# Kernel tuning notes

Hardware: AMD Instinct MI355X
Metric: run time of the kernel (lower is better)

Reference implementation:

```python
import jax, jax.numpy as jnp
import numpy as np

# bitsandbytes NF4 codebook (16 values)
NF4_TABLE = jnp.array([
    -1.0, -0.6961928009986877, -0.5250730514526367, -0.39491748809814453,
    -0.28444138169288635, -0.18477343022823334, -0.09105003625154495, 0.0,
    0.07958029955625534, 0.16093020141124725, 0.24611230194568634,
    0.33791524171829224, 0.44070982933044434, 0.5626170039176941,
    0.6989939212799072, 1.0], dtype=jnp.float32)
BLOCK = 64  # bitsandbytes default quantization blocksize


def dequant_nf4(codes, absmax):
    # codes: [out, in] int codebook indices; absmax: [out, in//BLOCK] per-block scales
    out_f, in_f = codes.shape
    w = NF4_TABLE[codes].reshape(out_f, in_f // BLOCK, BLOCK) * absmax[:, :, None]
    return w.reshape(out_f, in_f)


def setup_inputs() -> dict:
    key = jax.random.key(0)
    ks = jax.random.split(key, 7)
    dim, hidden = 4096, 11008
    B, S = 2, 2048
    x = jax.random.normal(ks[0], (B, S, dim), dtype=jnp.float32)
    w1_codes = jax.random.randint(ks[1], (hidden, dim), 0, 16, dtype=jnp.int32)
    w1_absmax = jax.random.uniform(ks[2], (hidden, dim // BLOCK), dtype=jnp.float32) * 0.05
    w2_codes = jax.random.randint(ks[3], (dim, hidden), 0, 16, dtype=jnp.int32)
    w2_absmax = jax.random.uniform(ks[4], (dim, hidden // BLOCK), dtype=jnp.float32) * 0.05
    w3_codes = jax.random.randint(ks[5], (hidden, dim), 0, 16, dtype=jnp.int32)
    w3_absmax = jax.random.uniform(ks[6], (hidden, dim // BLOCK), dtype=jnp.float32) * 0.05
    return {"x": x,
            "w1_codes": w1_codes, "w1_absmax": w1_absmax,
            "w2_codes": w2_codes, "w2_absmax": w2_absmax,
            "w3_codes": w3_codes, "w3_absmax": w3_absmax}


def reference(x, w1_codes, w1_absmax, w2_codes, w2_absmax, w3_codes, w3_absmax):
    # SwiGLU: w2(silu(w1(x)) * w3(x)) with NF4-dequantized weights, no bias
    W1 = dequant_nf4(w1_codes, w1_absmax)  # [hidden, dim]
    W3 = dequant_nf4(w3_codes, w3_absmax)  # [hidden, dim]
    W2 = dequant_nf4(w2_codes, w2_absmax)  # [dim, hidden]
    h = jax.nn.silu(jnp.einsum('bsd,hd->bsh', x, W1)) * jnp.einsum('bsd,hd->bsh', x, W3)
    return jnp.einsum('bsh,dh->bsd', h, W2)
```

## Files before the change

### kernel.cpp

```cpp
#include <hip/hip_runtime.h>
#include <hip/hip_bf16.h>
#include <stdint.h>

#define DIM   4096
#define HID   11008
#define MTOK  4096
#define NELW  (HID * DIM)

typedef __bf16 bf16x8 __attribute__((ext_vector_type(8)));
typedef float  f32x4  __attribute__((ext_vector_type(4)));
using gptr_t = const __attribute__((address_space(1))) void*;
using lptr_t = __attribute__((address_space(3))) void*;

__device__ __forceinline__ float bf2f(unsigned short u) {
    unsigned int t = ((unsigned int)u) << 16;
    float f; __builtin_memcpy(&f, &t, 4); return f;
}
__device__ __forceinline__ unsigned short f2bf(float f) {
    unsigned int x; __builtin_memcpy(&x, &f, 4);
    x += 0x7fffu + ((x >> 16) & 1u);
    return (unsigned short)(x >> 16);
}

__device__ __constant__ float NF4_TAB[16] = {
    -1.0f, -0.6961928009986877f, -0.5250730514526367f, -0.39491748809814453f,
    -0.28444138169288635f, -0.18477343022823334f, -0.09105003625154495f, 0.0f,
    0.07958029955625534f, 0.16093020141124725f, 0.24611230194568634f,
    0.33791524171829224f, 0.44070982933044434f, 0.5626170039176941f,
    0.6989939212799072f, 1.0f};

__global__ __launch_bounds__(256) void dequant_nf4_k(
    const int* __restrict__ codes, const float* __restrict__ absmax,
    unsigned short* __restrict__ out)
{
    long base = ((long)blockIdx.x * 256 + threadIdx.x) * 8;
    float tv = NF4_TAB[threadIdx.x & 15];
    int4 c0 = *(const int4*)(codes + base);
    int4 c1 = *(const int4*)(codes + base + 4);
    float s = absmax[base >> 6];
    union { uint4 q; unsigned short u[8]; } o;
    o.u[0] = f2bf(__shfl(tv, c0.x) * s);
    o.u[1] = f2bf(__shfl(tv, c0.y) * s);
    o.u[2] = f2bf(__shfl(tv, c0.z) * s);
    o.u[3] = f2bf(__shfl(tv, c0.w) * s);
    o.u[4] = f2bf(__shfl(tv, c1.x) * s);
    o.u[5] = f2bf(__shfl(tv, c1.y) * s);
    o.u[6] = f2bf(__shfl(tv, c1.z) * s);
    o.u[7] = f2bf(__shfl(tv, c1.w) * s);
    *(uint4*)(out + base) = o.q;
}

__global__ __launch_bounds__(256) void cast_f32_bf16_k(
    const float* __restrict__ in, unsigned short* __restrict__ out)
{
    long base = ((long)blockIdx.x * 256 + threadIdx.x) * 8;
    float4 a = *(const float4*)(in + base);
    float4 b = *(const float4*)(in + base + 4);
    union { uint4 q; unsigned short u[8]; } o;
    o.u[0] = f2bf(a.x); o.u[1] = f2bf(a.y); o.u[2] = f2bf(a.z); o.u[3] = f2bf(a.w);
    o.u[4] = f2bf(b.x); o.u[5] = f2bf(b.y); o.u[6] = f2bf(b.z); o.u[7] = f2bf(b.w);
    *(uint4*)(out + base) = o.q;
}

template<int MODE>
__global__ __launch_bounds__(512, 2) void gemm256_k(
    const unsigned short* __restrict__ A, const unsigned short* __restrict__ B,
    void* __restrict__ Cout, int M, int N, int K)
{
    __shared__ __align__(16) unsigned short lds[2][2][2][128 * 64];

    const int tid = threadIdx.x;
    const int w = tid >> 6, lane = tid & 63;
    const int wm = w >> 2, wn = w & 3;
    const int lrow = lane & 15, hi = lane >> 4;
    const int key = lrow & 7;

    const int nbm = M >> 8, nbn = N >> 8;
    const int cpx = (nbm * nbn) >> 3;
    int swz = ((int)blockIdx.x & 7) * cpx + ((int)blockIdx.x >> 3);
    const int bm = swz % nbm, bn = swz / nbm;

    const long ldK = K;
    const int srow = tid >> 3;
    const int scol = ((tid & 7) ^ (srow & 7)) * 8;
    const unsigned short* gA = A + ((long)(bm * 256 + srow)) * ldK + scol;
    const unsigned short* gB = B + ((long)(bn * 256 + srow)) * ldK + scol;

    f32x4 acc[8][4];
    #pragma unroll
    for (int m = 0; m < 8; ++m)
        #pragma unroll
        for (int n = 0; n < 4; ++n) acc[m][n] = f32x4{0.f, 0.f, 0.f, 0.f};

    bf16x8 a0[4][2], a1[4][2], b0[2][2], b1[2][2];

    auto STAGE = [&](int kt, int h, int b) {
        const unsigned short* src = ((h >> 1) ? gB : gA)
            + (long)((h & 1) * 128) * ldK + (long)kt * 64;
        char* dst = (char*)&lds[b][h >> 1][h & 1][0] + w * 1024;
        __builtin_amdgcn_global_load_lds((gptr_t)src, (lptr_t)dst, 16, 0, 0);
        __builtin_amdgcn_global_load_lds((gptr_t)(src + (long)64 * ldK),
                                         (lptr_t)(dst + 8192), 16, 0, 0);
    };
    auto LDA = [&](bf16x8 (&fr)[4][2], int which, int b) {
        const unsigned short* base = &lds[b][0][wm][0];
        #pragma unroll
        for (int m = 0; m < 4; ++m)
            #pragma unroll
            for (int ks = 0; ks < 2; ++ks)
                fr[m][ks] = *(const bf16x8*)(base + (which * 64 + m * 16 + lrow) * 64
                                             + (((ks * 4 + hi) ^ key) * 8));
    };
    auto LDB = [&](bf16x8 (&fr)[2][2], int which, int b) {
        const unsigned short* base = &lds[b][1][wn >> 1][0];
        #pragma unroll
        for (int n = 0; n < 2; ++n)
            #pragma unroll
            for (int ks = 0; ks < 2; ++ks)
                fr[n][ks] = *(const bf16x8*)(base + ((wn & 1) * 64 + (which * 2 + n) * 16 + lrow) * 64
                                             + (((ks * 4 + hi) ^ key) * 8));
    };
    auto MMA = [&](bf16x8 (&fa)[4][2], bf16x8 (&fb)[2][2], int mo, int no) {
        __builtin_amdgcn_s_setprio(1);
        #pragma unroll
        for (int m = 0; m < 4; ++m)
            #pragma unroll
            for (int n = 0; n < 2; ++n)
                #pragma unroll
                for (int ks = 0; ks < 2; ++ks)
                    acc[mo + m][no + n] = __builtin_amdgcn_mfma_f32_16x16x32_bf16(
                        fa[m][ks], fb[n][ks], acc[mo + m][no + n], 0, 0, 0);
        __builtin_amdgcn_s_setprio(0);
    };
    #define BAR() do { __builtin_amdgcn_s_barrier(); \
                       __builtin_amdgcn_sched_barrier(0xF); } while (0)

    const int NT = K >> 6;
    STAGE(0, 0, 0); STAGE(0, 1, 0); STAGE(0, 2, 0); STAGE(0, 3, 0);
    STAGE(1, 0, 1); STAGE(1, 1, 1);
    asm volatile("s_waitcnt vmcnt(4)" ::: "memory");
    BAR();
    LDA(a0, 0, 0);

    int cur = 0;
    for (int t = 0; t < NT - 1; ++t) {
        const int nb = cur ^ 1;
        const int tA = (t + 2 < NT) ? t + 2 : NT - 1;
        STAGE(t + 1, 2, nb);
        LDB(b0, 0, cur);
        BAR();
        MMA(a0, b0, 0, 0);
        BAR();
        STAGE(t + 1, 3, nb);
        LDA(a1, 1, cur);
        BAR();
        MMA(a1, b0, 4, 0);
        BAR();
        STAGE(tA, 0, cur);
        LDB(b1, 1, cur);
        BAR();
        MMA(a0, b1, 0, 2);
        asm volatile("s_waitcnt vmcnt(6)" ::: "memory");
        BAR();
        STAGE(tA, 1, cur);
        LDA(a0, 0, nb);
        BAR();
        MMA(a1, b1, 4, 2);
        asm volatile("s_waitcnt vmcnt(4)" ::: "memory");
        BAR();
        cur = nb;
    }
    LDB(b0, 0, cur);
    MMA(a0, b0, 0, 0);
    LDA(a1, 1, cur);
    MMA(a1, b0, 4, 0);
    LDB(b1, 1, cur);
    MMA(a0, b1, 0, 2);
    MMA(a1, b1, 4, 2);
    #undef BAR

    const int grow = bm * 256 + wm * 128 + hi * 4;
    const int gcol = bn * 256 + wn * 64 + lrow;
    if (MODE == 0) {
        float* C = (float*)Cout;
        #pragma unroll
        for (int m = 0; m < 8; ++m)
            #pragma unroll
            for (int n = 0; n < 4; ++n)
                #pragma unroll
                for (int r = 0; r < 4; ++r)
                    C[(long)(grow + m * 16 + r) * N + gcol + n * 16] = acc[m][n][r];
    } else if (MODE == 1) {
        unsigned short* C = (unsigned short*)Cout;
        #pragma unroll
        for (int m = 0; m < 8; ++m)
            #pragma unroll
            for (int n = 0; n < 4; ++n)
                #pragma unroll
                for (int r = 0; r < 4; ++r)
                    C[(long)(grow + m * 16 + r) * N + gcol + n * 16] = f2bf(acc[m][n][r]);
    } else {
        unsigned short* C = (unsigned short*)Cout;
        #pragma unroll
        for (int m = 0; m < 8; ++m)
            #pragma unroll
            for (int n = 0; n < 4; ++n)
                #pragma unroll
                for (int r = 0; r < 4; ++r) {
                    long idx = (long)(grow + m * 16 + r) * N + gcol + n * 16;
                    float h1v = bf2f(C[idx]);
                    float g = h1v / (1.0f + __expf(-h1v));
                    C[idx] = f2bf(g * acc[m][n][r]);
                }
    }
}

#define WS_NEEDED 304087040UL

extern "C" void kernel_launch(void* const* d_in, const int* in_sizes, int n_in,
                              void* d_out, int out_size, void* d_ws, size_t ws_size,
                              hipStream_t stream) {
    const float* x   = (const float*)d_in[0];
    const int*   w1c = (const int*)d_in[1];
    const float* w1a = (const float*)d_in[2];
    const int*   w2c = (const int*)d_in[3];
    const float* w2a = (const float*)d_in[4];
    const int*   w3c = (const int*)d_in[5];
    const float* w3a = (const float*)d_in[6];

    if (ws_size < WS_NEEDED) return;

    char* ws = (char*)d_ws;
    unsigned short* W1 = (unsigned short*)(ws);
    unsigned short* W3 = (unsigned short*)(ws + 90177536);
    unsigned short* Xb = (unsigned short*)(ws + 180355072);
    unsigned short* H1 = (unsigned short*)(ws + 213909504);

    const int wblk = NELW / (8 * 256);
    dequant_nf4_k<<<wblk, 256, 0, stream>>>(w1c, w1a, W1);
    dequant_nf4_k<<<wblk, 256, 0, stream>>>(w3c, w3a, W3);
    cast_f32_bf16_k<<<(MTOK * DIM) / (8 * 256), 256, 0, stream>>>(x, Xb);

    gemm256_k<1><<<(MTOK / 256) * (HID / 256), 512, 0, stream>>>(Xb, W1, H1, MTOK, HID, DIM);
    gemm256_k<2><<<(MTOK / 256) * (HID / 256), 512, 0, stream>>>(Xb, W3, H1, MTOK, HID, DIM);

    dequant_nf4_k<<<wblk, 256, 0, stream>>>(w2c, w2a, W1);

    gemm256_k<0><<<(MTOK / 256) * (DIM / 256), 512, 0, stream>>>(H1, W1, (float*)d_out, MTOK, DIM, HID);
}
```

Measured before the change: 1.165 ms.

## Use 32x32 MFMA tiles and overlap NF4 dequant with the GEMM grids

The GEMM inner loop moves from 16x16x32 to 32x32x16 bf16 MFMA instructions, with LDS fragment loads, accumulators and the epilogue row mapping rewritten to match. This cuts LDS reads per FLOP. The standalone W3 and W2 dequant launches are removed. Each is folded into the preceding GEMM launch as extra trailing grid-stride blocks, so the dequant runs alongside the GEMM tail instead of serially. The W1 dequant and the x-to-bf16 cast are merged into one launch. The risks are contention between dequant blocks and GEMM blocks, and correctness of the new 32x32 fragment layout.

```diff
diff --git a/kernel.cpp b/kernel.cpp
--- a/kernel.cpp
+++ b/kernel.cpp
@@ -8,7 +8,7 @@
 #define NELW  (HID * DIM)
 
 typedef __bf16 bf16x8 __attribute__((ext_vector_type(8)));
-typedef float  f32x4  __attribute__((ext_vector_type(4)));
+typedef float  f32x16 __attribute__((ext_vector_type(16)));
 using gptr_t = const __attribute__((address_space(1))) void*;
 using lptr_t = __attribute__((address_space(3))) void*;
 
@@ -29,12 +29,9 @@
     0.33791524171829224f, 0.44070982933044434f, 0.5626170039176941f,
     0.6989939212799072f, 1.0f};
 
-__global__ __launch_bounds__(256) void dequant_nf4_k(
-    const int* __restrict__ codes, const float* __restrict__ absmax,
-    unsigned short* __restrict__ out)
+__device__ __forceinline__ void dq8(const int* codes, const float* absmax,
+                                    unsigned short* out, long base, float tv)
 {
-    long base = ((long)blockIdx.x * 256 + threadIdx.x) * 8;
-    float tv = NF4_TAB[threadIdx.x & 15];
     int4 c0 = *(const int4*)(codes + base);
     int4 c1 = *(const int4*)(codes + base + 4);
     float s = absmax[base >> 6];
@@ -50,30 +47,55 @@
     *(uint4*)(out + base) = o.q;
 }
 
-__global__ __launch_bounds__(256) void cast_f32_bf16_k(
-    const float* __restrict__ in, unsigned short* __restrict__ out)
+#define W1BLK 22016
+#define PREBLK (W1BLK + (MTOK * DIM) / 2048)
+__global__ __launch_bounds__(256) void pre_k(
+    const int* __restrict__ w1c, const float* __restrict__ w1a,
+    unsigned short* __restrict__ W1,
+    const float* __restrict__ x, unsigned short* __restrict__ Xb)
 {
-    long base = ((long)blockIdx.x * 256 + threadIdx.x) * 8;
-    float4 a = *(const float4*)(in + base);
-    float4 b = *(const float4*)(in + base + 4);
-    union { uint4 q; unsigned short u[8]; } o;
-    o.u[0] = f2bf(a.x); o.u[1] = f2bf(a.y); o.u[2] = f2bf(a.z); o.u[3] = f2bf(a.w);
-    o.u[4] = f2bf(b.x); o.u[5] = f2bf(b.y); o.u[6] = f2bf(b.z); o.u[7] = f2bf(b.w);
-    *(uint4*)(out + base) = o.q;
+    float tv = NF4_TAB[threadIdx.x & 15];
+    if ((int)blockIdx.x < W1BLK) {
+        long base = ((long)blockIdx.x * 256 + threadIdx.x) * 8;
+        dq8(w1c, w1a, W1, base, tv);
+    } else {
+        long base = ((long)(blockIdx.x - W1BLK) * 256 + threadIdx.x) * 8;
+        float4 a = *(const float4*)(x + base);
+        float4 b = *(const float4*)(x + base + 4);
+        union { uint4 q; unsigned short u[8]; } o;
+        o.u[0] = f2bf(a.x); o.u[1] = f2bf(a.y); o.u[2] = f2bf(a.z); o.u[3] = f2bf(a.w);
+        o.u[4] = f2bf(b.x); o.u[5] = f2bf(b.y); o.u[6] = f2bf(b.z); o.u[7] = f2bf(b.w);
+        *(uint4*)(Xb + base) = o.q;
+    }
 }
 
 template<int MODE>
 __global__ __launch_bounds__(512, 2) void gemm256_k(
     const unsigned short* __restrict__ A, const unsigned short* __restrict__ B,
-    void* __restrict__ Cout, int M, int N, int K)
+    void* __restrict__ Cout, int M, int N, int K, int ngemm,
+    const int* __restrict__ dqc, const float* __restrict__ dqa,
+    unsigned short* __restrict__ dqo)
 {
     __shared__ __align__(16) unsigned short lds[2][2][2][128 * 64];
 
     const int tid = threadIdx.x;
-    const int w = tid >> 6, lane = tid & 63;
+    const int lane = tid & 63;
+
+    if ((int)blockIdx.x >= ngemm) {
+        if (!dqo) return;
+        const int b = (int)blockIdx.x - ngemm;
+        const int ndq = (int)gridDim.x - ngemm;
+        const long stride = (long)ndq * 512 * 8;
+        float tv = NF4_TAB[lane & 15];
+        for (long base = ((long)b * 512 + tid) * 8; base < (long)NELW; base += stride)
+            dq8(dqc, dqa, dqo, base, tv);
+        return;
+    }
+
+    const int w = tid >> 6;
     const int wm = w >> 2, wn = w & 3;
-    const int lrow = lane & 15, hi = lane >> 4;
-    const int key = lrow & 7;
+    const int l31 = lane & 31, l5 = lane >> 5;
+    const int key = lane & 7;
 
     const int nbm = M >> 8, nbn = N >> 8;
     const int cpx = (nbm * nbn) >> 3;
@@ -86,13 +108,15 @@
     const unsigned short* gA = A + ((long)(bm * 256 + srow)) * ldK + scol;
     const unsigned short* gB = B + ((long)(bn * 256 + srow)) * ldK + scol;
 
-    f32x4 acc[8][4];
+    f32x16 acc[4][2];
     #pragma unroll
-    for (int m = 0; m < 8; ++m)
-        #pragma unroll
-        for (int n = 0; n < 4; ++n) acc[m][n] = f32x4{0.f, 0.f, 0.f, 0.f};
-
-    bf16x8 a0[4][2], a1[4][2], b0[2][2], b1[2][2];
+    for (int m = 0; m < 4; ++m)
+        #pragma unroll
+        for (int n = 0; n < 2; ++n)
+            #pragma unroll
+            for (int r = 0; r < 16; ++r) acc[m][n][r] = 0.f;
+
+    bf16x8 aLo[2][4], aHi[2][4], bLo[4], bHi[4];
 
     auto STAGE = [&](int kt, int h, int b) {
         const unsigned short* src = ((h >> 1) ? gB : gA)
@@ -102,34 +126,34 @@
         __builtin_amdgcn_global_load_lds((gptr_t)(src + (long)64 * ldK),
                                          (lptr_t)(dst + 8192), 16, 0, 0);
     };
-    auto LDA = [&](bf16x8 (&fr)[4][2], int which, int b) {
+    auto LDA32 = [&](bf16x8 (&fr)[2][4], int which, int b) {
         const unsigned short* base = &lds[b][0][wm][0];
         #pragma unroll
-        for (int m = 0; m < 4; ++m)
-            #pragma unroll
-            for (int ks = 0; ks < 2; ++ks)
-                fr[m][ks] = *(const bf16x8*)(base + (which * 64 + m * 16 + lrow) * 64
-                                             + (((ks * 4 + hi) ^ key) * 8));
-    };
-    auto LDB = [&](bf16x8 (&fr)[2][2], int which, int b) {
+        for (int mt = 0; mt < 2; ++mt)
+            #pragma unroll
+            for (int ks = 0; ks < 4; ++ks) {
+                const int row = which * 64 + mt * 32 + l31;
+                fr[mt][ks] = *(const bf16x8*)(base + row * 64
+                                              + (((ks * 2 + l5) ^ key) * 8));
+            }
+    };
+    auto LDB32 = [&](bf16x8 (&fr)[4], int which, int b) {
         const unsigned short* base = &lds[b][1][wn >> 1][0];
         #pragma unroll
-        for (int n = 0; n < 2; ++n)
-            #pragma unroll
-            for (int ks = 0; ks < 2; ++ks)
-                fr[n][ks] = *(const bf16x8*)(base + ((wn & 1) * 64 + (which * 2 + n) * 16 + lrow) * 64
-                                             + (((ks * 4 + hi) ^ key) * 8));
-    };
-    auto MMA = [&](bf16x8 (&fa)[4][2], bf16x8 (&fb)[2][2], int mo, int no) {
+        for (int ks = 0; ks < 4; ++ks) {
+            const int row = (wn & 1) * 64 + which * 32 + l31;
+            fr[ks] = *(const bf16x8*)(base + row * 64
+                                      + (((ks * 2 + l5) ^ key) * 8));
+        }
+    };
+    auto MMA32 = [&](bf16x8 (&fa)[2][4], bf16x8 (&fb)[4], int mo, int no) {
         __builtin_amdgcn_s_setprio(1);
         #pragma unroll
-        for (int m = 0; m < 4; ++m)
-            #pragma unroll
-            for (int n = 0; n < 2; ++n)
-                #pragma unroll
-                for (int ks = 0; ks < 2; ++ks)
-                    acc[mo + m][no + n] = __builtin_amdgcn_mfma_f32_16x16x32_bf16(
-                        fa[m][ks], fb[n][ks], acc[mo + m][no + n], 0, 0, 0);
+        for (int mt = 0; mt < 2; ++mt)
+            #pragma unroll
+            for (int ks = 0; ks < 4; ++ks)
+                acc[mo + mt][no] = __builtin_amdgcn_mfma_f32_32x32x16_bf16(
+                    fa[mt][ks], fb[ks], acc[mo + mt][no], 0, 0, 0);
         __builtin_amdgcn_s_setprio(0);
     };
     #define BAR() do { __builtin_amdgcn_s_barrier(); \
@@ -140,82 +164,70 @@
     STAGE(1, 0, 1); STAGE(1, 1, 1);
     asm volatile("s_waitcnt vmcnt(4)" ::: "memory");
     BAR();
-    LDA(a0, 0, 0);
+    LDA32(aLo, 0, 0);
 
     int cur = 0;
     for (int t = 0; t < NT - 1; ++t) {
         const int nb = cur ^ 1;
         const int tA = (t + 2 < NT) ? t + 2 : NT - 1;
         STAGE(t + 1, 2, nb);
-        LDB(b0, 0, cur);
-        BAR();
-        MMA(a0, b0, 0, 0);
+        LDB32(bLo, 0, cur);
+        BAR();
+        MMA32(aLo, bLo, 0, 0);
         BAR();
         STAGE(t + 1, 3, nb);
-        LDA(a1, 1, cur);
-        BAR();
-        MMA(a1, b0, 4, 0);
+        LDA32(aHi, 1, cur);
+        BAR();
+        MMA32(aHi, bLo, 2, 0);
         BAR();
         STAGE(tA, 0, cur);
-        LDB(b1, 1, cur);
-        BAR();
-        MMA(a0, b1, 0, 2);
+        LDB32(bHi, 1, cur);
+        BAR();
+        MMA32(aLo, bHi, 0, 1);
         asm volatile("s_waitcnt vmcnt(6)" ::: "memory");
         BAR();
         STAGE(tA, 1, cur);
-        LDA(a0, 0, nb);
-        BAR();
-        MMA(a1, b1, 4, 2);
+        LDA32(aLo, 0, nb);
+        BAR();
+        MMA32(aHi, bHi, 2, 1);
         asm volatile("s_waitcnt vmcnt(4)" ::: "memory");
         BAR();
         cur = nb;
     }
-    LDB(b0, 0, cur);
-    MMA(a0, b0, 0, 0);
-    LDA(a1, 1, cur);
-    MMA(a1, b0, 4, 0);
-    LDB(b1, 1, cur);
-    MMA(a0, b1, 0, 2);
-    MMA(a1, b1, 4, 2);
+    LDB32(bLo, 0, cur);
+    MMA32(aLo, bLo, 0, 0);
+    LDA32(aHi, 1, cur);
+    MMA32(aHi, bLo, 2, 0);
+    LDB32(bHi, 1, cur);
+    MMA32(aLo, bHi, 0, 1);
+    MMA32(aHi, bHi, 2, 1);
     #undef BAR
 
-    const int grow = bm * 256 + wm * 128 + hi * 4;
-    const int gcol = bn * 256 + wn * 64 + lrow;
-    if (MODE == 0) {
-        float* C = (float*)Cout;
-        #pragma unroll
-        for (int m = 0; m < 8; ++m)
-            #pragma unroll
-            for (int n = 0; n < 4; ++n)
-                #pragma unroll
-                for (int r = 0; r < 4; ++r)
-                    C[(long)(grow + m * 16 + r) * N + gcol + n * 16] = acc[m][n][r];
-    } else if (MODE == 1) {
-        unsigned short* C = (unsigned short*)Cout;
-        #pragma unroll
-        for (int m = 0; m < 8; ++m)
-            #pragma unroll
-            for (int n = 0; n < 4; ++n)
-                #pragma unroll
-                for (int r = 0; r < 4; ++r)
-                    C[(long)(grow + m * 16 + r) * N + gcol + n * 16] = f2bf(acc[m][n][r]);
-    } else {
-        unsigned short* C = (unsigned short*)Cout;
-        #pragma unroll
-        for (int m = 0; m < 8; ++m)
-            #pragma unroll
-            for (int n = 0; n < 4; ++n)
-                #pragma unroll
-                for (int r = 0; r < 4; ++r) {
-                    long idx = (long)(grow + m * 16 + r) * N + gcol + n * 16;
+    const int grow0 = bm * 256 + wm * 128 + l5 * 4;
+    const int gcol0 = bn * 256 + wn * 64 + l31;
+    #pragma unroll
+    for (int mt = 0; mt < 4; ++mt)
+        #pragma unroll
+        for (int nt = 0; nt < 2; ++nt)
+            #pragma unroll
+            for (int r = 0; r < 16; ++r) {
+                const int row = grow0 + mt * 32 + (r & 3) + 8 * (r >> 2);
+                const long idx = (long)row * N + gcol0 + nt * 32;
+                if (MODE == 0) {
+                    ((float*)Cout)[idx] = acc[mt][nt][r];
+                } else if (MODE == 1) {
+                    ((unsigned short*)Cout)[idx] = f2bf(acc[mt][nt][r]);
+                } else {
+                    unsigned short* C = (unsigned short*)Cout;
                     float h1v = bf2f(C[idx]);
                     float g = h1v / (1.0f + __expf(-h1v));
-                    C[idx] = f2bf(g * acc[m][n][r]);
+                    C[idx] = f2bf(g * acc[mt][nt][r]);
                 }
-    }
+            }
 }
 
 #define WS_NEEDED 304087040UL
+#define DQBLK 512
 
 extern "C" void kernel_launch(void* const* d_in, const int* in_sizes, int n_in,
                               void* d_out, int out_size, void* d_ws, size_t ws_size,
@@ -236,15 +248,15 @@
     unsigned short* Xb = (unsigned short*)(ws + 180355072);
     unsigned short* H1 = (unsigned short*)(ws + 213909504);
 
-    const int wblk = NELW / (8 * 256);
-    dequant_nf4_k<<<wblk, 256, 0, stream>>>(w1c, w1a, W1);
-    dequant_nf4_k<<<wblk, 256, 0, stream>>>(w3c, w3a, W3);
-    cast_f32_bf16_k<<<(MTOK * DIM) / (8 * 256), 256, 0, stream>>>(x, Xb);
-
-    gemm256_k<1><<<(MTOK / 256) * (HID / 256), 512, 0, stream>>>(Xb, W1, H1, MTOK, HID, DIM);
-    gemm256_k<2><<<(MTOK / 256) * (HID / 256), 512, 0, stream>>>(Xb, W3, H1, MTOK, HID, DIM);
-
-    dequant_nf4_k<<<wblk, 256, 0, stream>>>(w2c, w2a, W1);
-
-    gemm256_k<0><<<(MTOK / 256) * (DIM / 256), 512, 0, stream>>>(H1, W1, (float*)d_out, MTOK, DIM, HID);
-}
+    pre_k<<<PREBLK, 256, 0, stream>>>(w1c, w1a, W1, x, Xb);
+
+    const int g12 = (MTOK / 256) * (HID / 256);
+    const int g3  = (MTOK / 256) * (DIM / 256);
+
+    gemm256_k<1><<<g12 + DQBLK, 512, 0, stream>>>(Xb, W1, H1, MTOK, HID, DIM,
+                                                  g12, w3c, w3a, W3);
+    gemm256_k<2><<<g12 + DQBLK, 512, 0, stream>>>(Xb, W3, H1, MTOK, HID, DIM,
+                                                  g12, w2c, w2a, W1);
+    gemm256_k<0><<<g3, 512, 0, stream>>>(H1, W1, (float*)d_out, MTOK, DIM, HID,
+                                         g3, nullptr, nullptr, nullptr);
+}
```

Measured after the change: 1.291 ms. 1.11x slower.

## Overlap next weight dequantization with GEMM tail blocks and merge prologue kernels

Applied to the files above, without the earlier changes.

Appends 512 extra blocks to each of the first two GEMM grids. These blocks dequantize the weights the next GEMM needs (W3 during the W1 GEMM, W2 during the W3 GEMM), so that work fills the partially idle last wave of GEMM blocks instead of running as separate bandwidth-bound kernels. The W1 dequant and the x-to-bf16 cast are merged into a single prologue launch. The extra blocks compete with GEMM blocks for memory bandwidth and CU slots, and correctness depends on buffer reuse ordering being safe across launches.

```diff
diff --git a/kernel.cpp b/kernel.cpp
--- a/kernel.cpp
+++ b/kernel.cpp
@@ -29,12 +29,9 @@
     0.33791524171829224f, 0.44070982933044434f, 0.5626170039176941f,
     0.6989939212799072f, 1.0f};
 
-__global__ __launch_bounds__(256) void dequant_nf4_k(
-    const int* __restrict__ codes, const float* __restrict__ absmax,
-    unsigned short* __restrict__ out)
+__device__ __forceinline__ void dq8(const int* codes, const float* absmax,
+                                    unsigned short* out, long base, float tv)
 {
-    long base = ((long)blockIdx.x * 256 + threadIdx.x) * 8;
-    float tv = NF4_TAB[threadIdx.x & 15];
     int4 c0 = *(const int4*)(codes + base);
     int4 c1 = *(const int4*)(codes + base + 4);
     float s = absmax[base >> 6];
@@ -50,27 +47,52 @@
     *(uint4*)(out + base) = o.q;
 }
 
-__global__ __launch_bounds__(256) void cast_f32_bf16_k(
-    const float* __restrict__ in, unsigned short* __restrict__ out)
+#define W1BLK 22016
+#define PREBLK (W1BLK + (MTOK * DIM) / 2048)
+__global__ __launch_bounds__(256) void pre_k(
+    const int* __restrict__ w1c, const float* __restrict__ w1a,
+    unsigned short* __restrict__ W1,
+    const float* __restrict__ x, unsigned short* __restrict__ Xb)
 {
-    long base = ((long)blockIdx.x * 256 + threadIdx.x) * 8;
-    float4 a = *(const float4*)(in + base);
-    float4 b = *(const float4*)(in + base + 4);
-    union { uint4 q; unsigned short u[8]; } o;
-    o.u[0] = f2bf(a.x); o.u[1] = f2bf(a.y); o.u[2] = f2bf(a.z); o.u[3] = f2bf(a.w);
-    o.u[4] = f2bf(b.x); o.u[5] = f2bf(b.y); o.u[6] = f2bf(b.z); o.u[7] = f2bf(b.w);
-    *(uint4*)(out + base) = o.q;
+    float tv = NF4_TAB[threadIdx.x & 15];
+    if ((int)blockIdx.x < W1BLK) {
+        long base = ((long)blockIdx.x * 256 + threadIdx.x) * 8;
+        dq8(w1c, w1a, W1, base, tv);
+    } else {
+        long base = ((long)(blockIdx.x - W1BLK) * 256 + threadIdx.x) * 8;
+        float4 a = *(const float4*)(x + base);
+        float4 b = *(const float4*)(x + base + 4);
+        union { uint4 q; unsigned short u[8]; } o;
+        o.u[0] = f2bf(a.x); o.u[1] = f2bf(a.y); o.u[2] = f2bf(a.z); o.u[3] = f2bf(a.w);
+        o.u[4] = f2bf(b.x); o.u[5] = f2bf(b.y); o.u[6] = f2bf(b.z); o.u[7] = f2bf(b.w);
+        *(uint4*)(Xb + base) = o.q;
+    }
 }
 
 template<int MODE>
 __global__ __launch_bounds__(512, 2) void gemm256_k(
     const unsigned short* __restrict__ A, const unsigned short* __restrict__ B,
-    void* __restrict__ Cout, int M, int N, int K)
+    void* __restrict__ Cout, int M, int N, int K, int ngemm,
+    const int* __restrict__ dqc, const float* __restrict__ dqa,
+    unsigned short* __restrict__ dqo)
 {
     __shared__ __align__(16) unsigned short lds[2][2][2][128 * 64];
 
     const int tid = threadIdx.x;
-    const int w = tid >> 6, lane = tid & 63;
+    const int lane = tid & 63;
+
+    if ((int)blockIdx.x >= ngemm) {
+        if (!dqo) return;
+        const int b = (int)blockIdx.x - ngemm;
+        const int ndq = (int)gridDim.x - ngemm;
+        const long stride = (long)ndq * 512 * 8;
+        float tv = NF4_TAB[lane & 15];
+        for (long base = ((long)b * 512 + tid) * 8; base < (long)NELW; base += stride)
+            dq8(dqc, dqa, dqo, base, tv);
+        return;
+    }
+
+    const int w = tid >> 6;
     const int wm = w >> 2, wn = w & 3;
     const int lrow = lane & 15, hi = lane >> 4;
     const int key = lrow & 7;
@@ -216,6 +238,7 @@
 }
 
 #define WS_NEEDED 304087040UL
+#define DQBLK 512
 
 extern "C" void kernel_launch(void* const* d_in, const int* in_sizes, int n_in,
                               void* d_out, int out_size, void* d_ws, size_t ws_size,
@@ -236,15 +259,15 @@
     unsigned short* Xb = (unsigned short*)(ws + 180355072);
     unsigned short* H1 = (unsigned short*)(ws + 213909504);
 
-    const int wblk = NELW / (8 * 256);
-    dequant_nf4_k<<<wblk, 256, 0, stream>>>(w1c, w1a, W1);
-    dequant_nf4_k<<<wblk, 256, 0, stream>>>(w3c, w3a, W3);
-    cast_f32_bf16_k<<<(MTOK * DIM) / (8 * 256), 256, 0, stream>>>(x, Xb);
-
-    gemm256_k<1><<<(MTOK / 256) * (HID / 256), 512, 0, stream>>>(Xb, W1, H1, MTOK, HID, DIM);
-    gemm256_k<2><<<(MTOK / 256) * (HID / 256), 512, 0, stream>>>(Xb, W3, H1, MTOK, HID, DIM);
-
-    dequant_nf4_k<<<wblk, 256, 0, stream>>>(w2c, w2a, W1);
-
-    gemm256_k<0><<<(MTOK / 256) * (DIM / 256), 512, 0, stream>>>(H1, W1, (float*)d_out, MTOK, DIM, HID);
-}
+    pre_k<<<PREBLK, 256, 0, stream>>>(w1c, w1a, W1, x, Xb);
+
+    const int g12 = (MTOK / 256) * (HID / 256);
+    const int g3  = (MTOK / 256) * (DIM / 256);
+
+    gemm256_k<1><<<g12 + DQBLK, 512, 0, stream>>>(Xb, W1, H1, MTOK, HID, DIM,
+                                                  g12, w3c, w3a, W3);
+    gemm256_k<2><<<g12 + DQBLK, 512, 0, stream>>>(Xb, W3, H1, MTOK, HID, DIM,
+                                                  g12, w2c, w2a, W1);
+    gemm256_k<0><<<g3, 512, 0, stream>>>(H1, W1, (float*)d_out, MTOK, DIM, HID,
+                                         g3, nullptr, nullptr, nullptr);
+}
```

After: 1.135 ms. 1.03x faster.
